# Kernel tuning notes

Hardware: AMD Instinct MI355X
Metric: run time of the kernel (lower is better)

## Reference

```python
import jax, jax.numpy as jnp
import numpy as np

DIM = 64
HEADS = 4
SHAPE = (2, 64, 64, 64, DIM)  # [n, h, w, d, C] channels-last


def setup_inputs() -> dict:
    key = jax.random.key(0)
    ks = jax.random.split(key, 9)
    s = 1.0 / np.sqrt(DIM)
    return {
        "x": jax.random.normal(ks[0], SHAPE, dtype=jnp.float32),
        "Wk": jax.random.normal(ks[1], (DIM, DIM), dtype=jnp.float32) * s,
        "bk": jax.random.normal(ks[2], (DIM,), dtype=jnp.float32) * 0.01,
        "Wq": jax.random.normal(ks[3], (DIM, DIM), dtype=jnp.float32) * s,
        "bq": jax.random.normal(ks[4], (DIM,), dtype=jnp.float32) * 0.01,
        "Wv": jax.random.normal(ks[5], (DIM, DIM), dtype=jnp.float32) * s,
        "bv": jax.random.normal(ks[6], (DIM,), dtype=jnp.float32) * 0.01,
        "Wr": jax.random.normal(ks[7], (DIM, DIM), dtype=jnp.float32) * s,
        "br": jax.random.normal(ks[8], (DIM,), dtype=jnp.float32) * 0.01,
        "head_count": HEADS,
    }


def reference(x, Wk, bk, Wq, bq, Wv, bv, Wr, br, head_count):
    n, h, w, d, C = x.shape
    N = h * w * d
    H = head_count
    dk = C // H  # head key channels == head value channels (key/value channels = dim)

    xf = x.reshape(n, N, C)  # tokens along flattened spatial axis
    # Conv3d with 1x1x1 kernel == per-token linear projection over channels
    k = xf @ Wk.T + bk  # [n, N, C]
    q = xf @ Wq.T + bq
    v = xf @ Wv.T + bv

    # split channels into contiguous head chunks -> [n, H, dk, N]
    k = k.reshape(n, N, H, dk).transpose(0, 2, 3, 1)
    q = q.reshape(n, N, H, dk).transpose(0, 2, 3, 1)
    v = v.reshape(n, N, H, dk).transpose(0, 2, 3, 1)

    k = jax.nn.softmax(k, axis=3)  # softmax over spatial positions
    q = jax.nn.softmax(q, axis=2)  # softmax over head key channels

    # context = softmax(K) @ V^T : [n, H, dk, dv]
    ctx = jnp.einsum('nhkN,nhvN->nhkv', k, v)
    # attended = context^T @ softmax(Q) : [n, H, dv, N]
    att = jnp.einsum('nhkv,nhkN->nhvN', ctx, q)

    agg = att.transpose(0, 3, 1, 2).reshape(n, N, C)  # concat heads on channels
    out = agg @ Wr.T + br  # reprojection (1x1x1 conv)
    return out.reshape(n, h, w, d, C)
```

## Files before the change

kernel.cpp:

```cpp
#include <hip/hip_runtime.h>
#include <math.h>


#define NTOK 262144
typedef float4 f4;
typedef _Float16 f16;
typedef __attribute__((ext_vector_type(8))) _Float16 f16x8;
typedef __attribute__((ext_vector_type(4))) _Float16 f16x4;
typedef __attribute__((ext_vector_type(4))) float f32x4;

#define WS_S  0
#define WS_Z  2048
#define WS_MH 2176

__device__ __forceinline__ f16x8 cvt8h2(f4 a, f4 b) {
    f16x8 r;
    r[0] = (f16)a.x; r[1] = (f16)a.y; r[2] = (f16)a.z; r[3] = (f16)a.w;
    r[4] = (f16)b.x; r[5] = (f16)b.y; r[6] = (f16)b.z; r[7] = (f16)b.w;
    return r;
}

__global__ __launch_bounds__(256) void k_init(float* __restrict__ ws) {
    int i = blockIdx.x * 256 + threadIdx.x;
    if (i < 2176) ws[i] = 0.0f;
}

__global__ __launch_bounds__(256) void k_ctx(const float* __restrict__ x,
                                             const float* __restrict__ Wk,
                                             const float* __restrict__ bk,
                                             const float* __restrict__ Wv,
                                             const float* __restrict__ bv,
                                             float* __restrict__ ws) {
    __shared__ __align__(16) char smem[40960];
    f16 (*ekb)[16][40] = (f16(*)[16][40])smem;
    f16 (*evb)[16][40] = (f16(*)[16][40])(smem + 20480);

    const int tid  = threadIdx.x;
    const int w    = tid >> 6;
    const int lane = tid & 63;
    const int lr   = lane & 15;
    const int ql   = lane >> 4;

    const int nb = blockIdx.x >> 9;
    const int bi = blockIdx.x & 511;
    const long base = (long)nb * NTOK + (long)bi * 512 + (long)w * 128;

    f16x8 wkf[4][2], wvf[4][2];
    float bks[4], bvs[4];
    #pragma unroll
    for (int h = 0; h < 4; ++h) {
        const float* kr = &Wk[(16 * h + lr) * 64 + 8 * ql];
        const float* vr = &Wv[(16 * h + lr) * 64 + 8 * ql];
        #pragma unroll
        for (int jc = 0; jc < 2; ++jc) {
            wkf[h][jc] = cvt8h2(*(const f4*)&kr[32 * jc], *(const f4*)&kr[32 * jc + 4]);
            wvf[h][jc] = cvt8h2(*(const f4*)&vr[32 * jc], *(const f4*)&vr[32 * jc + 4]);
        }
        bks[h] = bk[16 * h + lr];
        bvs[h] = bv[16 * h + lr];
    }

    const f32x4 zero4 = {0.f, 0.f, 0.f, 0.f};
    f32x4 S[4] = {zero4, zero4, zero4, zero4};
    float z[4] = {0.f, 0.f, 0.f, 0.f};

    f4 L0, L1, L2, L3;
    {
        const float* xp = x + (((size_t)(base + lr)) << 6) + 8 * ql;
        L0 = *(const f4*)xp;        L1 = *(const f4*)(xp + 4);
        L2 = *(const f4*)(xp + 32); L3 = *(const f4*)(xp + 36);
    }

    for (int ch = 0; ch < 4; ++ch) {
        #pragma unroll
        for (int s = 0; s < 2; ++s) {
            f16x8 a0 = cvt8h2(L0, L1), a1 = cvt8h2(L2, L3);
            const int nxt = ch * 2 + s + 1;
            if (nxt < 8) {
                const float* xp = x + (((size_t)(base + nxt * 16 + lr)) << 6) + 8 * ql;
                L0 = *(const f4*)xp;        L1 = *(const f4*)(xp + 4);
                L2 = *(const f4*)(xp + 32); L3 = *(const f4*)(xp + 36);
            }
            #pragma unroll
            for (int h = 0; h < 4; ++h) {
                f32x4 ak = zero4, av = zero4;
                ak = __builtin_amdgcn_mfma_f32_16x16x32_f16(a0, wkf[h][0], ak, 0, 0, 0);
                ak = __builtin_amdgcn_mfma_f32_16x16x32_f16(a1, wkf[h][1], ak, 0, 0, 0);
                av = __builtin_amdgcn_mfma_f32_16x16x32_f16(a0, wvf[h][0], av, 0, 0, 0);
                av = __builtin_amdgcn_mfma_f32_16x16x32_f16(a1, wvf[h][1], av, 0, 0, 0);
                const float e0 = __expf(ak[0] + bks[h]), e1 = __expf(ak[1] + bks[h]);
                const float e2 = __expf(ak[2] + bks[h]), e3 = __expf(ak[3] + bks[h]);
                z[h] += (e0 + e1) + (e2 + e3);
                f16x4 pk = {(f16)e0, (f16)e1, (f16)e2, (f16)e3};
                f16x4 pv = {(f16)(av[0] + bvs[h]), (f16)(av[1] + bvs[h]),
                            (f16)(av[2] + bvs[h]), (f16)(av[3] + bvs[h])};
                *(f16x4*)&ekb[w * 4 + h][lr][s * 16 + 4 * ql] = pk;
                *(f16x4*)&evb[w * 4 + h][lr][s * 16 + 4 * ql] = pv;
            }
        }
        #pragma unroll
        for (int h = 0; h < 4; ++h) {
            f16x8 ekf = *(f16x8*)&ekb[w * 4 + h][lr][8 * ql];
            f16x8 evf = *(f16x8*)&evb[w * 4 + h][lr][8 * ql];
            S[h] = __builtin_amdgcn_mfma_f32_16x16x32_f16(ekf, evf, S[h], 0, 0, 0);
        }
    }

    #pragma unroll
    for (int h = 0; h < 4; ++h) {
        z[h] += __shfl_xor(z[h], 16);
        z[h] += __shfl_xor(z[h], 32);
    }

    __syncthreads();
    float* sr = (float*)smem;
    float* zr = (float*)(smem + 16384);
    #pragma unroll
    for (int h = 0; h < 4; ++h) {
        #pragma unroll
        for (int r = 0; r < 4; ++r)
            sr[((w * 4 + h) * 16 + 4 * ql + r) * 16 + lr] = S[h][r];
        if (lane < 16) zr[(w * 4 + h) * 16 + lane] = z[h];
    }
    __syncthreads();
    #pragma unroll
    for (int i = 0; i < 4; ++i) {
        const int idx = i * 256 + tid;
        const float acc = sr[idx] + sr[1024 + idx] + sr[2048 + idx] + sr[3072 + idx];
        atomicAdd(&ws[WS_S + nb * 1024 + idx], acc);
    }
    if (tid < 64) {
        const float acc = zr[tid] + zr[64 + tid] + zr[128 + tid] + zr[192 + tid];
        atomicAdd(&ws[WS_Z + nb * 64 + tid], acc);
    }
}

__global__ __launch_bounds__(256) void k_m(const float* __restrict__ Wr,
                                           float* __restrict__ ws) {
    const int n = blockIdx.x;
    f16* MH = (f16*)(ws + WS_MH);
    for (int i = threadIdx.x; i < 4096; i += 256) {
        const int c = i >> 6, p = i & 63;
        const int h = p >> 4, kc = p & 15;
        const float rz = 1.0f / ws[WS_Z + n * 64 + p];
        const float* Srow = ws + WS_S + n * 1024 + h * 256 + kc * 16;
        const float* Wrow = Wr + c * 64 + h * 16;
        float acc = 0.f;
        #pragma unroll
        for (int vc = 0; vc < 16; ++vc) acc += Wrow[vc] * Srow[vc];
        MH[n * 4096 + c * 64 + p] = (f16)(acc * rz);
    }
}

__global__ __launch_bounds__(256) void k_out(const float* __restrict__ x,
                                             const float* __restrict__ Wq,
                                             const float* __restrict__ bq,
                                             const float* __restrict__ br,
                                             float* __restrict__ out,
                                             const float* __restrict__ ws) {
    __shared__ f16 qb[4][16][72];

    const int tid  = threadIdx.x;
    const int w    = tid >> 6;
    const int lane = tid & 63;
    const int lr   = lane & 15;
    const int ql   = lane >> 4;

    const int nb = blockIdx.x >> 10;
    const int bi = blockIdx.x & 1023;
    const long base = (long)nb * NTOK + (long)bi * 256 + (long)w * 64;

    f16x8 wqf[4][2];
    f4 bqv[4];
    #pragma unroll
    for (int h = 0; h < 4; ++h) {
        const float* qr = &Wq[(16 * h + lr) * 64 + 8 * ql];
        #pragma unroll
        for (int jc = 0; jc < 2; ++jc)
            wqf[h][jc] = cvt8h2(*(const f4*)&qr[32 * jc], *(const f4*)&qr[32 * jc + 4]);
        bqv[h] = *(const f4*)&bq[16 * h + 4 * ql];
    }
    f16x8 mf[4][2];
    f4 brv[4];
    const f16* MH = (const f16*)(ws + WS_MH) + (size_t)nb * 4096;
    #pragma unroll
    for (int oc = 0; oc < 4; ++oc) {
        #pragma unroll
        for (int pc = 0; pc < 2; ++pc)
            mf[oc][pc] = *(const f16x8*)&MH[(16 * oc + lr) * 64 + 32 * pc + 8 * ql];
        brv[oc] = *(const f4*)&br[16 * oc + 4 * ql];
    }

    const f32x4 zero4 = {0.f, 0.f, 0.f, 0.f};
    const int sw = (lr & 3) << 4;

    f4 L0, L1, L2, L3;
    {
        const float* xp = x + (((size_t)(base + lr)) << 6) + 8 * ql;
        L0 = *(const f4*)xp;        L1 = *(const f4*)(xp + 4);
        L2 = *(const f4*)(xp + 32); L3 = *(const f4*)(xp + 36);
    }

    for (int s = 0; s < 4; ++s) {
        f16x8 b0 = cvt8h2(L0, L1), b1 = cvt8h2(L2, L3);
        if (s < 3) {
            const float* xp = x + (((size_t)(base + (s + 1) * 16 + lr)) << 6) + 8 * ql;
            L0 = *(const f4*)xp;        L1 = *(const f4*)(xp + 4);
            L2 = *(const f4*)(xp + 32); L3 = *(const f4*)(xp + 36);
        }
        #pragma unroll
        for (int h = 0; h < 4; ++h) {
            f32x4 aq = zero4;
            aq = __builtin_amdgcn_mfma_f32_16x16x32_f16(wqf[h][0], b0, aq, 0, 0, 0);
            aq = __builtin_amdgcn_mfma_f32_16x16x32_f16(wqf[h][1], b1, aq, 0, 0, 0);
            float q0 = aq[0] + bqv[h].x, q1 = aq[1] + bqv[h].y;
            float q2 = aq[2] + bqv[h].z, q3 = aq[3] + bqv[h].w;
            float mx = fmaxf(fmaxf(q0, q1), fmaxf(q2, q3));
            mx = fmaxf(mx, __shfl_xor(mx, 16));
            mx = fmaxf(mx, __shfl_xor(mx, 32));
            float e0 = __expf(q0 - mx), e1 = __expf(q1 - mx);
            float e2 = __expf(q2 - mx), e3 = __expf(q3 - mx);
            float sm = (e0 + e1) + (e2 + e3);
            sm += __shfl_xor(sm, 16);
            sm += __shfl_xor(sm, 32);
            const float rs = 1.0f / sm;
            f16x4 ph = {(f16)(e0 * rs), (f16)(e1 * rs), (f16)(e2 * rs), (f16)(e3 * rs)};
            *(f16x4*)&qb[w][lr][16 * (h ^ (lr & 3)) + 4 * ql] = ph;
        }
        f16x8 qv0 = *(f16x8*)&qb[w][lr][(8 * ql) ^ sw];
        f16x8 qv1 = *(f16x8*)&qb[w][lr][(32 + 8 * ql) ^ sw];
        const size_t obase = ((size_t)(base + s * 16 + lr)) << 6;
        #pragma unroll
        for (int oc = 0; oc < 4; ++oc) {
            f32x4 o = zero4;
            o = __builtin_amdgcn_mfma_f32_16x16x32_f16(mf[oc][0], qv0, o, 0, 0, 0);
            o = __builtin_amdgcn_mfma_f32_16x16x32_f16(mf[oc][1], qv1, o, 0, 0, 0);
            const f4 res = {o[0] + brv[oc].x, o[1] + brv[oc].y,
                            o[2] + brv[oc].z, o[3] + brv[oc].w};
            *(f4*)&out[obase + 16 * oc + 4 * ql] = res;
        }
    }
}

extern "C" void kernel_launch(void* const* d_in, const int* in_sizes, int n_in,
                              void* d_out, int out_size, void* d_ws, size_t ws_size,
                              hipStream_t stream) {
    const float* x  = (const float*)d_in[0];
    const float* Wk = (const float*)d_in[1];
    const float* bk = (const float*)d_in[2];
    const float* Wq = (const float*)d_in[3];
    const float* bq = (const float*)d_in[4];
    const float* Wv = (const float*)d_in[5];
    const float* bv = (const float*)d_in[6];
    const float* Wr = (const float*)d_in[7];
    const float* br = (const float*)d_in[8];
    float* out = (float*)d_out;
    float* ws  = (float*)d_ws;

    hipLaunchKernelGGL(k_init, dim3(9),    dim3(256), 0, stream, ws);
    hipLaunchKernelGGL(k_ctx,  dim3(1024), dim3(256), 0, stream, x, Wk, bk, Wv, bv, ws);
    hipLaunchKernelGGL(k_m,    dim3(2),    dim3(256), 0, stream, Wr, ws);
    hipLaunchKernelGGL(k_out,  dim3(2048), dim3(256), 0, stream, x, Wq, bq, br, out, ws);
}
```

Baseline: 124.8 us.

## Feed MFMA outputs directly as 16x16x16 operands, fold biases algebraically, drop LDS staging

```diff
diff --git a/kernel.cpp b/kernel.cpp
--- a/kernel.cpp
+++ b/kernel.cpp
@@ -25,15 +25,12 @@
     if (i < 2176) ws[i] = 0.0f;
 }
 
-__global__ __launch_bounds__(256) void k_ctx(const float* __restrict__ x,
-                                             const float* __restrict__ Wk,
-                                             const float* __restrict__ bk,
-                                             const float* __restrict__ Wv,
-                                             const float* __restrict__ bv,
-                                             float* __restrict__ ws) {
-    __shared__ __align__(16) char smem[40960];
-    f16 (*ekb)[16][40] = (f16(*)[16][40])smem;
-    f16 (*evb)[16][40] = (f16(*)[16][40])(smem + 20480);
+__global__ __launch_bounds__(256, 4) void k_ctx(const float* __restrict__ x,
+                                                const float* __restrict__ Wk,
+                                                const float* __restrict__ Wv,
+                                                float* __restrict__ ws) {
+    __shared__ float sr[4096];
+    __shared__ float zr[256];
 
     const int tid  = threadIdx.x;
     const int w    = tid >> 6;
@@ -46,7 +43,6 @@
     const long base = (long)nb * NTOK + (long)bi * 512 + (long)w * 128;
 
     f16x8 wkf[4][2], wvf[4][2];
-    float bks[4], bvs[4];
     #pragma unroll
     for (int h = 0; h < 4; ++h) {
         const float* kr = &Wk[(16 * h + lr) * 64 + 8 * ql];
@@ -56,8 +52,6 @@
             wkf[h][jc] = cvt8h2(*(const f4*)&kr[32 * jc], *(const f4*)&kr[32 * jc + 4]);
             wvf[h][jc] = cvt8h2(*(const f4*)&vr[32 * jc], *(const f4*)&vr[32 * jc + 4]);
         }
-        bks[h] = bk[16 * h + lr];
-        bvs[h] = bv[16 * h + lr];
     }
 
     const f32x4 zero4 = {0.f, 0.f, 0.f, 0.f};
@@ -71,38 +65,26 @@
         L2 = *(const f4*)(xp + 32); L3 = *(const f4*)(xp + 36);
     }
 
-    for (int ch = 0; ch < 4; ++ch) {
-        #pragma unroll
-        for (int s = 0; s < 2; ++s) {
-            f16x8 a0 = cvt8h2(L0, L1), a1 = cvt8h2(L2, L3);
-            const int nxt = ch * 2 + s + 1;
-            if (nxt < 8) {
-                const float* xp = x + (((size_t)(base + nxt * 16 + lr)) << 6) + 8 * ql;
-                L0 = *(const f4*)xp;        L1 = *(const f4*)(xp + 4);
-                L2 = *(const f4*)(xp + 32); L3 = *(const f4*)(xp + 36);
-            }
-            #pragma unroll
-            for (int h = 0; h < 4; ++h) {
-                f32x4 ak = zero4, av = zero4;
-                ak = __builtin_amdgcn_mfma_f32_16x16x32_f16(a0, wkf[h][0], ak, 0, 0, 0);
-                ak = __builtin_amdgcn_mfma_f32_16x16x32_f16(a1, wkf[h][1], ak, 0, 0, 0);
-                av = __builtin_amdgcn_mfma_f32_16x16x32_f16(a0, wvf[h][0], av, 0, 0, 0);
-                av = __builtin_amdgcn_mfma_f32_16x16x32_f16(a1, wvf[h][1], av, 0, 0, 0);
-                const float e0 = __expf(ak[0] + bks[h]), e1 = __expf(ak[1] + bks[h]);
-                const float e2 = __expf(ak[2] + bks[h]), e3 = __expf(ak[3] + bks[h]);
-                z[h] += (e0 + e1) + (e2 + e3);
-                f16x4 pk = {(f16)e0, (f16)e1, (f16)e2, (f16)e3};
-                f16x4 pv = {(f16)(av[0] + bvs[h]), (f16)(av[1] + bvs[h]),
-                            (f16)(av[2] + bvs[h]), (f16)(av[3] + bvs[h])};
-                *(f16x4*)&ekb[w * 4 + h][lr][s * 16 + 4 * ql] = pk;
-                *(f16x4*)&evb[w * 4 + h][lr][s * 16 + 4 * ql] = pv;
-            }
+    for (int s = 0; s < 8; ++s) {
+        f16x8 a0 = cvt8h2(L0, L1), a1 = cvt8h2(L2, L3);
+        if (s < 7) {
+            const float* xp = x + (((size_t)(base + (s + 1) * 16 + lr)) << 6) + 8 * ql;
+            L0 = *(const f4*)xp;        L1 = *(const f4*)(xp + 4);
+            L2 = *(const f4*)(xp + 32); L3 = *(const f4*)(xp + 36);
         }
         #pragma unroll
         for (int h = 0; h < 4; ++h) {
-            f16x8 ekf = *(f16x8*)&ekb[w * 4 + h][lr][8 * ql];
-            f16x8 evf = *(f16x8*)&evb[w * 4 + h][lr][8 * ql];
-            S[h] = __builtin_amdgcn_mfma_f32_16x16x32_f16(ekf, evf, S[h], 0, 0, 0);
+            f32x4 ak = zero4, av = zero4;
+            ak = __builtin_amdgcn_mfma_f32_16x16x32_f16(a0, wkf[h][0], ak, 0, 0, 0);
+            ak = __builtin_amdgcn_mfma_f32_16x16x32_f16(a1, wkf[h][1], ak, 0, 0, 0);
+            av = __builtin_amdgcn_mfma_f32_16x16x32_f16(a0, wvf[h][0], av, 0, 0, 0);
+            av = __builtin_amdgcn_mfma_f32_16x16x32_f16(a1, wvf[h][1], av, 0, 0, 0);
+            const float e0 = __expf(ak[0]), e1 = __expf(ak[1]);
+            const float e2 = __expf(ak[2]), e3 = __expf(ak[3]);
+            z[h] += (e0 + e1) + (e2 + e3);
+            f16x4 ekf = {(f16)e0, (f16)e1, (f16)e2, (f16)e3};
+            f16x4 evf = {(f16)av[0], (f16)av[1], (f16)av[2], (f16)av[3]};
+            S[h] = __builtin_amdgcn_mfma_f32_16x16x16f16(ekf, evf, S[h], 0, 0, 0);
         }
     }
 
@@ -112,9 +94,6 @@
         z[h] += __shfl_xor(z[h], 32);
     }
 
-    __syncthreads();
-    float* sr = (float*)smem;
-    float* zr = (float*)(smem + 16384);
     #pragma unroll
     for (int h = 0; h < 4; ++h) {
         #pragma unroll
@@ -136,6 +115,7 @@
 }
 
 __global__ __launch_bounds__(256) void k_m(const float* __restrict__ Wr,
+                                           const float* __restrict__ bv,
                                            float* __restrict__ ws) {
     const int n = blockIdx.x;
     f16* MH = (f16*)(ws + WS_MH);
@@ -145,21 +125,23 @@
         const float rz = 1.0f / ws[WS_Z + n * 64 + p];
         const float* Srow = ws + WS_S + n * 1024 + h * 256 + kc * 16;
         const float* Wrow = Wr + c * 64 + h * 16;
-        float acc = 0.f;
-        #pragma unroll
-        for (int vc = 0; vc < 16; ++vc) acc += Wrow[vc] * Srow[vc];
-        MH[n * 4096 + c * 64 + p] = (f16)(acc * rz);
-    }
-}
-
-__global__ __launch_bounds__(256) void k_out(const float* __restrict__ x,
-                                             const float* __restrict__ Wq,
-                                             const float* __restrict__ bq,
-                                             const float* __restrict__ br,
-                                             float* __restrict__ out,
-                                             const float* __restrict__ ws) {
-    __shared__ f16 qb[4][16][72];
-
+        const float* bvr  = bv + h * 16;
+        float acc = 0.f, accb = 0.f;
+        #pragma unroll
+        for (int vc = 0; vc < 16; ++vc) {
+            acc  += Wrow[vc] * Srow[vc];
+            accb += Wrow[vc] * bvr[vc];
+        }
+        MH[n * 4096 + c * 64 + p] = (f16)(acc * rz + accb);
+    }
+}
+
+__global__ __launch_bounds__(256, 4) void k_out(const float* __restrict__ x,
+                                                const float* __restrict__ Wq,
+                                                const float* __restrict__ bq,
+                                                const float* __restrict__ br,
+                                                float* __restrict__ out,
+                                                const float* __restrict__ ws) {
     const int tid  = threadIdx.x;
     const int w    = tid >> 6;
     const int lane = tid & 63;
@@ -171,28 +153,31 @@
     const long base = (long)nb * NTOK + (long)bi * 256 + (long)w * 64;
 
     f16x8 wqf[4][2];
-    f4 bqv[4];
+    f16x4 bqh[4];
     #pragma unroll
     for (int h = 0; h < 4; ++h) {
         const float* qr = &Wq[(16 * h + lr) * 64 + 8 * ql];
         #pragma unroll
         for (int jc = 0; jc < 2; ++jc)
             wqf[h][jc] = cvt8h2(*(const f4*)&qr[32 * jc], *(const f4*)&qr[32 * jc + 4]);
-        bqv[h] = *(const f4*)&bq[16 * h + 4 * ql];
-    }
-    f16x8 mf[4][2];
-    f4 brv[4];
+        const f4 b = *(const f4*)&bq[16 * h + 4 * ql];
+        bqh[h][0] = (f16)b.x; bqh[h][1] = (f16)b.y;
+        bqh[h][2] = (f16)b.z; bqh[h][3] = (f16)b.w;
+    }
+    f16x4 mfa[4][4];
+    f16x4 brh[4];
     const f16* MH = (const f16*)(ws + WS_MH) + (size_t)nb * 4096;
     #pragma unroll
-    for (int oc = 0; oc < 4; ++oc) {
-        #pragma unroll
-        for (int pc = 0; pc < 2; ++pc)
-            mf[oc][pc] = *(const f16x8*)&MH[(16 * oc + lr) * 64 + 32 * pc + 8 * ql];
-        brv[oc] = *(const f4*)&br[16 * oc + 4 * ql];
+    for (int oct = 0; oct < 4; ++oct) {
+        #pragma unroll
+        for (int pc = 0; pc < 4; ++pc)
+            mfa[oct][pc] = *(const f16x4*)&MH[(16 * oct + lr) * 64 + 16 * pc + 4 * ql];
+        const f4 b = *(const f4*)&br[16 * oct + 4 * ql];
+        brh[oct][0] = (f16)b.x; brh[oct][1] = (f16)b.y;
+        brh[oct][2] = (f16)b.z; brh[oct][3] = (f16)b.w;
     }
 
     const f32x4 zero4 = {0.f, 0.f, 0.f, 0.f};
-    const int sw = (lr & 3) << 4;
 
     f4 L0, L1, L2, L3;
     {
@@ -208,13 +193,14 @@
             L0 = *(const f4*)xp;        L1 = *(const f4*)(xp + 4);
             L2 = *(const f4*)(xp + 32); L3 = *(const f4*)(xp + 36);
         }
+        f16x4 qf[4];
         #pragma unroll
         for (int h = 0; h < 4; ++h) {
             f32x4 aq = zero4;
             aq = __builtin_amdgcn_mfma_f32_16x16x32_f16(wqf[h][0], b0, aq, 0, 0, 0);
             aq = __builtin_amdgcn_mfma_f32_16x16x32_f16(wqf[h][1], b1, aq, 0, 0, 0);
-            float q0 = aq[0] + bqv[h].x, q1 = aq[1] + bqv[h].y;
-            float q2 = aq[2] + bqv[h].z, q3 = aq[3] + bqv[h].w;
+            float q0 = aq[0] + (float)bqh[h][0], q1 = aq[1] + (float)bqh[h][1];
+            float q2 = aq[2] + (float)bqh[h][2], q3 = aq[3] + (float)bqh[h][3];
             float mx = fmaxf(fmaxf(q0, q1), fmaxf(q2, q3));
             mx = fmaxf(mx, __shfl_xor(mx, 16));
             mx = fmaxf(mx, __shfl_xor(mx, 32));
@@ -224,20 +210,19 @@
             sm += __shfl_xor(sm, 16);
             sm += __shfl_xor(sm, 32);
             const float rs = 1.0f / sm;
-            f16x4 ph = {(f16)(e0 * rs), (f16)(e1 * rs), (f16)(e2 * rs), (f16)(e3 * rs)};
-            *(f16x4*)&qb[w][lr][16 * (h ^ (lr & 3)) + 4 * ql] = ph;
-        }
-        f16x8 qv0 = *(f16x8*)&qb[w][lr][(8 * ql) ^ sw];
-        f16x8 qv1 = *(f16x8*)&qb[w][lr][(32 + 8 * ql) ^ sw];
+            qf[h][0] = (f16)(e0 * rs); qf[h][1] = (f16)(e1 * rs);
+            qf[h][2] = (f16)(e2 * rs); qf[h][3] = (f16)(e3 * rs);
+        }
         const size_t obase = ((size_t)(base + s * 16 + lr)) << 6;
         #pragma unroll
-        for (int oc = 0; oc < 4; ++oc) {
+        for (int oct = 0; oct < 4; ++oct) {
             f32x4 o = zero4;
-            o = __builtin_amdgcn_mfma_f32_16x16x32_f16(mf[oc][0], qv0, o, 0, 0, 0);
-            o = __builtin_amdgcn_mfma_f32_16x16x32_f16(mf[oc][1], qv1, o, 0, 0, 0);
-            const f4 res = {o[0] + brv[oc].x, o[1] + brv[oc].y,
-                            o[2] + brv[oc].z, o[3] + brv[oc].w};
-            *(f4*)&out[obase + 16 * oc + 4 * ql] = res;
+            #pragma unroll
+            for (int pc = 0; pc < 4; ++pc)
+                o = __builtin_amdgcn_mfma_f32_16x16x16f16(mfa[oct][pc], qf[pc], o, 0, 0, 0);
+            const f4 res = {o[0] + (float)brh[oct][0], o[1] + (float)brh[oct][1],
+                            o[2] + (float)brh[oct][2], o[3] + (float)brh[oct][3]};
+            *(f4*)&out[obase + 16 * oct + 4 * ql] = res;
         }
     }
 }
@@ -247,7 +232,6 @@
                               hipStream_t stream) {
     const float* x  = (const float*)d_in[0];
     const float* Wk = (const float*)d_in[1];
-    const float* bk = (const float*)d_in[2];
     const float* Wq = (const float*)d_in[3];
     const float* bq = (const float*)d_in[4];
     const float* Wv = (const float*)d_in[5];
@@ -258,7 +242,7 @@
     float* ws  = (float*)d_ws;
 
     hipLaunchKernelGGL(k_init, dim3(9),    dim3(256), 0, stream, ws);
-    hipLaunchKernelGGL(k_ctx,  dim3(1024), dim3(256), 0, stream, x, Wk, bk, Wv, bv, ws);
-    hipLaunchKernelGGL(k_m,    dim3(2),    dim3(256), 0, stream, Wr, ws);
+    hipLaunchKernelGGL(k_ctx,  dim3(1024), dim3(256), 0, stream, x, Wk, Wv, ws);
+    hipLaunchKernelGGL(k_m,    dim3(2),    dim3(256), 0, stream, Wr, bv, ws);
     hipLaunchKernelGGL(k_out,  dim3(2048), dim3(256), 0, stream, x, Wq, bq, br, out, ws);
 }
```

New measurement: 125.4 us. No clear change (+0.5%).
